# Kernel optimization log

Hardware: AMD Instinct MI355X
Metric: run time of the kernel (lower is better)

## Reference

```python
import jax, jax.numpy as jnp
import numpy as np
from jax import lax

N = 50000
E = 320000
IN_DIM = 128
OUT_DIM = 64
N_CHANNEL = 8
KERNEL = 3
N_REL = 500
BN_EPS = 1e-5


def setup_inputs() -> dict:
    key = jax.random.key(0)
    ks = jax.random.split(key, 10)
    inp = jax.random.normal(ks[0], (N, IN_DIM), dtype=jnp.float32)
    heads = jax.random.randint(ks[1], (E,), 0, N)
    rels = jax.random.randint(ks[2], (E,), 0, N_REL)
    tails = jax.random.randint(ks[3], (E,), 0, N)
    triple = jnp.stack([heads, rels, tails], axis=1).astype(jnp.int64)
    # parameters
    limit_W = float(np.sqrt(6.0 / (IN_DIM + OUT_DIM)))  # xavier_uniform
    W = jax.random.uniform(ks[4], (IN_DIM, OUT_DIM), minval=-limit_W, maxval=limit_W, dtype=jnp.float32)
    rel_embed = jax.random.normal(ks[5], (N_REL, OUT_DIM), dtype=jnp.float32)
    fan_in = 1 * KERNEL * KERNEL
    b = float(1.0 / np.sqrt(fan_in))
    conv_w = jax.random.uniform(ks[6], (N_CHANNEL, 1, KERNEL, KERNEL), minval=-b, maxval=b, dtype=jnp.float32)
    conv_b = jax.random.uniform(ks[7], (N_CHANNEL,), minval=-b, maxval=b, dtype=jnp.float32)
    fc_in = N_CHANNEL * (OUT_DIM - KERNEL + 1) * (3 - KERNEL + 1)
    bf = float(1.0 / np.sqrt(fc_in))
    fc_w = jax.random.uniform(ks[8], (1, fc_in), minval=-bf, maxval=bf, dtype=jnp.float32)
    bn1_gamma = jnp.ones((1,), jnp.float32)
    bn1_beta = jnp.zeros((1,), jnp.float32)
    bn2_gamma = jnp.ones((N_CHANNEL,), jnp.float32)
    bn2_beta = jnp.zeros((N_CHANNEL,), jnp.float32)
    return {"input": inp, "triple": triple, "W": W, "rel_embed": rel_embed,
            "conv_w": conv_w, "conv_b": conv_b, "fc_w": fc_w,
            "bn1_gamma": bn1_gamma, "bn1_beta": bn1_beta,
            "bn2_gamma": bn2_gamma, "bn2_beta": bn2_beta}


def _bn_eval(x, gamma, beta):
    # eval-mode BatchNorm with running_mean=0, running_var=1
    scale = gamma / jnp.sqrt(1.0 + BN_EPS)
    return x * scale.reshape(1, -1, 1, 1) + beta.reshape(1, -1, 1, 1)


def reference(input, triple, W, rel_embed, conv_w, conv_b, fc_w,
              bn1_gamma, bn1_beta, bn2_gamma, bn2_beta):
    n = input.shape[0]
    inp = input @ W                       # [N, out_dim]
    head = triple[:, 0]
    tail = triple[:, 2]
    h = inp[head]                         # [E, D]
    r = rel_embed[triple[:, 1]]           # [E, D]
    t = inp[tail]                         # [E, D]
    # energy function: [E,1,D,3] -> bn1 -> conv -> bn2 -> relu -> fc
    x = jnp.stack([h, r, t], axis=-1)[:, None, :, :]   # [E,1,D,3]
    x = _bn_eval(x, bn1_gamma, bn1_beta)
    y = lax.conv_general_dilated(x, conv_w, (1, 1), 'VALID',
                                 dimension_numbers=('NCHW', 'OIHW', 'NCHW'))
    y = y + conv_b.reshape(1, -1, 1, 1)                 # [E,C,D-2,1]
    y = jax.nn.relu(_bn_eval(y, bn2_gamma, bn2_beta))
    y = y.reshape(y.shape[0], -1)
    e = y @ fc_w[0]                                     # [E]
    e = jax.nn.leaky_relu(e, 0.01)
    # sparse softmax over rows (head) then sparse mm with input_
    m = jax.ops.segment_max(e, head, num_segments=n)
    ex = jnp.exp(e - m[head])
    denom = jax.ops.segment_sum(ex, head, num_segments=n)
    attn = ex / denom[head]
    agg = jax.ops.segment_sum(attn[:, None] * t, head, num_segments=n)
    return jax.nn.elu(agg + inp)
```

## Files before the change

kernel.cpp:

```cpp
#include <hip/hip_runtime.h>
#include <hip/hip_bf16.h>
#include <stdint.h>

#define IN_DIM   128
#define OUT_DIM  64
#define NCH      8
#define N_REL    500
#define BN_EPS   1e-5f
#define CAP      32


#define KEEP(x) asm volatile("" : "+v"(x))

__device__ __forceinline__ float dpp_shl1(float x) {
    return __int_as_float(__builtin_amdgcn_update_dpp(
        0, __float_as_int(x), 0x130, 0xf, 0xf, true));
}

__device__ __forceinline__ void fold_cw_thread(
    const float* __restrict__ conv_w, const float* __restrict__ conv_b,
    const float* __restrict__ bn1g, const float* __restrict__ bn1b,
    const float* __restrict__ bn2g, const float* __restrict__ bn2b,
    float* __restrict__ cw, int c)
{
    if (c >= NCH) return;
    float rs  = rsqrtf(1.f + BN_EPS);
    float s1  = bn1g[0] * rs;
    float be1 = bn1b[0];
    float s2  = bn2g[c] * rs;
    float k1  = s1 * s2;
    float wsum = 0.f;
    for (int d = 0; d < 3; ++d) {
        float a  = conv_w[c * 9 + d * 3 + 0];
        float b  = conv_w[c * 9 + d * 3 + 1];
        float cc = conv_w[c * 9 + d * 3 + 2];
        wsum += a + b + cc;
        cw[c * 3 + d]      = k1 * a;
        cw[24 + c * 3 + d] = k1 * b;
        cw[48 + c * 3 + d] = k1 * cc;
    }
    cw[72 + c] = (be1 * wsum + conv_b[c]) * s2 + bn2b[c];
}

__global__ __launch_bounds__(256) void k_build(
    const float* __restrict__ X, const float* __restrict__ W,
    const int* __restrict__ triple,
    const float* __restrict__ conv_w, const float* __restrict__ conv_b,
    const float* __restrict__ bn1g, const float* __restrict__ bn1b,
    const float* __restrict__ bn2g, const float* __restrict__ bn2b,
    float* __restrict__ inp, int* __restrict__ cnt, int2* __restrict__ rt32,
    float* __restrict__ cw, int E, int N, int ngemm)
{
    __shared__ float Wl[IN_DIM * OUT_DIM];
    __shared__ float Xl[32 * IN_DIM];

    if ((int)blockIdx.x < ngemm) {
        const int rows0 = blockIdx.x * 32;
        const float4* W4 = (const float4*)W;
        for (int i = threadIdx.x; i < IN_DIM * OUT_DIM / 4; i += 256)
            ((float4*)Wl)[i] = W4[i];
        for (int i = threadIdx.x; i < 32 * IN_DIM / 4; i += 256) {
            int r = i >> 5, k4 = i & 31;
            int rr = rows0 + r;
            float4 v = make_float4(0.f, 0.f, 0.f, 0.f);
            if (rr < N) v = ((const float4*)X)[(unsigned)rr * (IN_DIM / 4) + k4];
            ((float4*)Xl)[i] = v;
        }
        __syncthreads();

        const int w = threadIdx.x >> 6;
        const int c = threadIdx.x & 63;
        float acc[8];
        #pragma unroll
        for (int r = 0; r < 8; ++r) acc[r] = 0.f;

        for (int k4 = 0; k4 < IN_DIM / 4; ++k4) {
            int k = k4 * 4;
            float w0 = Wl[(k + 0) * OUT_DIM + c];
            float w1 = Wl[(k + 1) * OUT_DIM + c];
            float w2 = Wl[(k + 2) * OUT_DIM + c];
            float w3 = Wl[(k + 3) * OUT_DIM + c];
            #pragma unroll
            for (int r = 0; r < 8; ++r) {
                const float4 x = *(const float4*)&Xl[(w * 8 + r) * IN_DIM + k];
                acc[r] = fmaf(x.w, w3, fmaf(x.z, w2, fmaf(x.y, w1, fmaf(x.x, w0, acc[r]))));
            }
        }
        #pragma unroll
        for (int r = 0; r < 8; ++r) {
            int rr = rows0 + w * 8 + r;
            if (rr < N) inp[(unsigned)rr * OUT_DIM + c] = acc[r];
        }
    } else {
        const int bb   = blockIdx.x - ngemm;
        const int gtid = bb * 256 + threadIdx.x;
        if (bb == 0 && threadIdx.x < NCH)
            fold_cw_thread(conv_w, conv_b, bn1g, bn1b, bn2g, bn2b, cw, threadIdx.x);
        if (gtid < E) {
            int j = gtid;
            int h = triple[3 * j], r = triple[3 * j + 1], t = triple[3 * j + 2];
            h = min(max(h, 0), N - 1);
            r = min(max(r, 0), N_REL - 1);
            t = min(max(t, 0), N - 1);
            int pos = atomicAdd(&cnt[h], 1);
            if (pos < CAP) rt32[(unsigned)h * CAP + pos] = make_int2(r, t);
        }
    }
}

__device__ __forceinline__ float dpp_wave_sum(float x) {
    x += __int_as_float(__builtin_amdgcn_update_dpp(0, __float_as_int(x), 0x111, 0xf, 0xf, true));
    x += __int_as_float(__builtin_amdgcn_update_dpp(0, __float_as_int(x), 0x112, 0xf, 0xf, true));
    x += __int_as_float(__builtin_amdgcn_update_dpp(0, __float_as_int(x), 0x114, 0xf, 0xf, true));
    x += __int_as_float(__builtin_amdgcn_update_dpp(0, __float_as_int(x), 0x118, 0xf, 0xf, true));
    x += __int_as_float(__builtin_amdgcn_update_dpp(0, __float_as_int(x), 0x142, 0xf, 0xf, true));
    x += __int_as_float(__builtin_amdgcn_update_dpp(0, __float_as_int(x), 0x143, 0xf, 0xf, true));
    return __int_as_float(__builtin_amdgcn_readlane(__float_as_int(x), 63));
}

__global__ __launch_bounds__(256) void k_fused_all(
    const float* __restrict__ inp, const float* __restrict__ rel_embed,
    const float* __restrict__ cw, const float* __restrict__ fc_w,
    const int* __restrict__ cnt, const int2* __restrict__ rt32,
    float* __restrict__ out, int N)
{
    const int lane   = threadIdx.x & 63;
    const int wave   = (blockIdx.x * (blockDim.x >> 6)) + (threadIdx.x >> 6);
    const int nwaves = gridDim.x * (blockDim.x >> 6);

    float fcl[NCH];
    #pragma unroll
    for (int c = 0; c < NCH; ++c) {
        fcl[c] = (lane < 62) ? fc_w[c * 62 + lane] : 0.f;
        KEEP(fcl[c]);
    }

    for (int h = wave; h < N; h += nwaves) {
        const int deg = min(cnt[h], CAP);

        float h0 = inp[(unsigned)h * OUT_DIM + lane];
        float h1 = dpp_shl1(h0);
        float h2 = dpp_shl1(h1);
        float Ht[NCH];
        #pragma unroll
        for (int c = 0; c < NCH; ++c) {
            float v = cw[72 + c];
            v = fmaf(cw[c * 3 + 0], h0, v);
            v = fmaf(cw[c * 3 + 1], h1, v);
            v = fmaf(cw[c * 3 + 2], h2, v);
            Ht[c] = v;
            KEEP(Ht[c]);
        }

        float m_run = -INFINITY, l_run = 0.f, agg = 0.f;
        int2 rtv = make_int2(0, 0);
        if (lane < deg) rtv = rt32[(unsigned)h * CAP + lane];

        if (deg > 0) {
            int rk = __builtin_amdgcn_readlane(rtv.x, 0);
            int tk = __builtin_amdgcn_readlane(rtv.y, 0);
            float rr = rel_embed[(unsigned)rk * OUT_DIM + lane];
            float tt = inp      [(unsigned)tk * OUT_DIM + lane];

            for (int k = 0; k < deg; ++k) {
                int rk1 = __builtin_amdgcn_readlane(rtv.x, k + 1);
                int tk1 = __builtin_amdgcn_readlane(rtv.y, k + 1);
                float rrN = rel_embed[(unsigned)rk1 * OUT_DIM + lane];
                float ttN = inp      [(unsigned)tk1 * OUT_DIM + lane];

                float r1 = dpp_shl1(rr), r2 = dpp_shl1(r1);
                float t1 = dpp_shl1(tt), t2 = dpp_shl1(t1);

                float acc = 0.f;
                #pragma unroll
                for (int c = 0; c < NCH; ++c) {
                    float y = Ht[c];
                    y = fmaf(cw[24 + c * 3 + 0], rr, y);
                    y = fmaf(cw[24 + c * 3 + 1], r1, y);
                    y = fmaf(cw[24 + c * 3 + 2], r2, y);
                    y = fmaf(cw[48 + c * 3 + 0], tt, y);
                    y = fmaf(cw[48 + c * 3 + 1], t1, y);
                    y = fmaf(cw[48 + c * 3 + 2], t2, y);
                    acc = fmaf(fmaxf(y, 0.f), fcl[c], acc);
                }
                float s  = dpp_wave_sum(acc);
                float ev = fmaxf(s, 0.01f * s);

                float mn = fmaxf(m_run, ev);
                float sc = __expf(m_run - mn);
                float wk = __expf(ev - mn);
                agg   = fmaf(agg, sc, wk * tt);
                l_run = fmaf(l_run, sc, wk);
                m_run = mn;

                rr = rrN; tt = ttN;
            }
        }
        float aggn = (l_run > 0.f) ? agg / l_run : 0.f;
        float x = aggn + h0;
        float y = x > 0.f ? x : (__expf(x) - 1.f);
        out[(unsigned)h * OUT_DIM + lane] = y;
    }
}

extern "C" void kernel_launch(void* const* d_in, const int* in_sizes, int n_in,
                              void* d_out, int out_size, void* d_ws, size_t ws_size,
                              hipStream_t stream)
{
    const float* input     = (const float*)d_in[0];
    const int*   triple    = (const int*)d_in[1];
    const float* W         = (const float*)d_in[2];
    const float* rel_embed = (const float*)d_in[3];
    const float* conv_w    = (const float*)d_in[4];
    const float* conv_b    = (const float*)d_in[5];
    const float* fc_w      = (const float*)d_in[6];
    const float* bn1g      = (const float*)d_in[7];
    const float* bn1b      = (const float*)d_in[8];
    const float* bn2g      = (const float*)d_in[9];
    const float* bn2b      = (const float*)d_in[10];
    float*       out       = (float*)d_out;

    const int N = in_sizes[0] / IN_DIM;
    const int E = in_sizes[1] / 3;

    auto align = [](size_t x) { return (x + 255) & ~(size_t)255; };
    char* base = (char*)d_ws;
    size_t o = 0;
    float* inp  = (float*)(base + o); o = align(o + (size_t)N * OUT_DIM * 4);
    int2*  rt32 = (int2*)(base + o);  o = align(o + (size_t)N * CAP * 8);
    float* cw   = (float*)(base + o); o = align(o + 80 * 4);
    int*   cnt  = (int*)(base + o);   o = align(o + (size_t)N * 4);

    hipMemsetAsync(cnt, 0, (size_t)N * 4, stream);

    const int ngemm   = (N + 31) / 32;
    const int nbucket = (E + 255) / 256;
    k_build<<<ngemm + nbucket, 256, 0, stream>>>(
        input, W, triple, conv_w, conv_b, bn1g, bn1b, bn2g, bn2b,
        inp, cnt, rt32, cw, E, N, ngemm);

    const int nblk = (N + 3) / 4;
    k_fused_all<<<nblk, 256, 0, stream>>>(inp, rel_embed, cw, fc_w,
                                          cnt, rt32, out, N);
}
```

Before: 197.2 us.

## Precompute per-relation conv contributions table and double-buffer edge loads

Adds extra blocks to the build kernel that precompute, for each of the 500 relations, the 8-channel conv response of the relation embedding, so the edge loop no longer does 24 FMAs and 2 DPP shifts per edge for the relation column. The fused kernel instead reads two float4 values per lane from this 1 MB table. Conv weights are hoisted into scalar registers once per wave, and the edge loop is reworked into a two-slot software pipeline with two accumulators. Each edge now reads 8x more relation data, though the table is small enough to likely stay in cache, and register pressure rises.

```diff
diff --git a/kernel.cpp b/kernel.cpp
--- a/kernel.cpp
+++ b/kernel.cpp
@@ -15,6 +15,10 @@
 __device__ __forceinline__ float dpp_shl1(float x) {
     return __int_as_float(__builtin_amdgcn_update_dpp(
         0, __float_as_int(x), 0x130, 0xf, 0xf, true));
+}
+
+__device__ __forceinline__ float sget(float x) {
+    return __int_as_float(__builtin_amdgcn_readfirstlane(__float_as_int(x)));
 }
 
 __device__ __forceinline__ void fold_cw_thread(
@@ -44,12 +48,13 @@
 
 __global__ __launch_bounds__(256) void k_build(
     const float* __restrict__ X, const float* __restrict__ W,
-    const int* __restrict__ triple,
+    const int* __restrict__ triple, const float* __restrict__ rel_embed,
     const float* __restrict__ conv_w, const float* __restrict__ conv_b,
     const float* __restrict__ bn1g, const float* __restrict__ bn1b,
     const float* __restrict__ bn2g, const float* __restrict__ bn2b,
     float* __restrict__ inp, int* __restrict__ cnt, int2* __restrict__ rt32,
-    float* __restrict__ cw, int E, int N, int ngemm)
+    float* __restrict__ cw, float* __restrict__ Rt,
+    int E, int N, int ngemm, int nbucket)
 {
     __shared__ float Wl[IN_DIM * OUT_DIM];
     __shared__ float Xl[32 * IN_DIM];
@@ -91,7 +96,7 @@
             int rr = rows0 + w * 8 + r;
             if (rr < N) inp[(unsigned)rr * OUT_DIM + c] = acc[r];
         }
-    } else {
+    } else if ((int)blockIdx.x < ngemm + nbucket) {
         const int bb   = blockIdx.x - ngemm;
         const int gtid = bb * 256 + threadIdx.x;
         if (bb == 0 && threadIdx.x < NCH)
@@ -105,6 +110,28 @@
             int pos = atomicAdd(&cnt[h], 1);
             if (pos < CAP) rt32[(unsigned)h * CAP + pos] = make_int2(r, t);
         }
+    } else {
+        const int rb  = blockIdx.x - ngemm - nbucket;
+        const int ln  = threadIdx.x & 63;
+        const int rel = rb * 4 + (threadIdx.x >> 6);
+        if (rel < N_REL) {
+            float rr = rel_embed[(unsigned)rel * OUT_DIM + ln];
+            float r1 = dpp_shl1(rr), r2 = dpp_shl1(r1);
+            float rs = rsqrtf(1.f + BN_EPS);
+            float s1 = bn1g[0] * rs;
+            float q[NCH];
+            #pragma unroll
+            for (int c = 0; c < NCH; ++c) {
+                float k1 = s1 * (bn2g[c] * rs);
+                float b0 = k1 * conv_w[c * 9 + 1];
+                float b1 = k1 * conv_w[c * 9 + 4];
+                float b2 = k1 * conv_w[c * 9 + 7];
+                q[c] = fmaf(b0, rr, fmaf(b1, r1, b2 * r2));
+            }
+            float4* dst = (float4*)&Rt[(unsigned)rel * (OUT_DIM * NCH) + ln * NCH];
+            dst[0] = make_float4(q[0], q[1], q[2], q[3]);
+            dst[1] = make_float4(q[4], q[5], q[6], q[7]);
+        }
     }
 }
 
@@ -119,7 +146,7 @@
 }
 
 __global__ __launch_bounds__(256) void k_fused_all(
-    const float* __restrict__ inp, const float* __restrict__ rel_embed,
+    const float* __restrict__ inp, const float* __restrict__ Rt,
     const float* __restrict__ cw, const float* __restrict__ fc_w,
     const int* __restrict__ cnt, const int2* __restrict__ rt32,
     float* __restrict__ out, int N)
@@ -127,6 +154,18 @@
     const int lane   = threadIdx.x & 63;
     const int wave   = (blockIdx.x * (blockDim.x >> 6)) + (threadIdx.x >> 6);
     const int nwaves = gridDim.x * (blockDim.x >> 6);
+
+    float cA0[NCH], cA1[NCH], cA2[NCH], cC0[NCH], cC1[NCH], cC2[NCH], k0c[NCH];
+    #pragma unroll
+    for (int c = 0; c < NCH; ++c) {
+        cA0[c] = sget(cw[c * 3 + 0]);
+        cA1[c] = sget(cw[c * 3 + 1]);
+        cA2[c] = sget(cw[c * 3 + 2]);
+        cC0[c] = sget(cw[48 + c * 3 + 0]);
+        cC1[c] = sget(cw[48 + c * 3 + 1]);
+        cC2[c] = sget(cw[48 + c * 3 + 2]);
+        k0c[c] = sget(cw[72 + c]);
+    }
 
     float fcl[NCH];
     #pragma unroll
@@ -144,10 +183,10 @@
         float Ht[NCH];
         #pragma unroll
         for (int c = 0; c < NCH; ++c) {
-            float v = cw[72 + c];
-            v = fmaf(cw[c * 3 + 0], h0, v);
-            v = fmaf(cw[c * 3 + 1], h1, v);
-            v = fmaf(cw[c * 3 + 2], h2, v);
+            float v = k0c[c];
+            v = fmaf(cA0[c], h0, v);
+            v = fmaf(cA1[c], h1, v);
+            v = fmaf(cA2[c], h2, v);
             Ht[c] = v;
             KEEP(Ht[c]);
         }
@@ -157,44 +196,54 @@
         if (lane < deg) rtv = rt32[(unsigned)h * CAP + lane];
 
         if (deg > 0) {
-            int rk = __builtin_amdgcn_readlane(rtv.x, 0);
-            int tk = __builtin_amdgcn_readlane(rtv.y, 0);
-            float rr = rel_embed[(unsigned)rk * OUT_DIM + lane];
-            float tt = inp      [(unsigned)tk * OUT_DIM + lane];
-
-            for (int k = 0; k < deg; ++k) {
-                int rk1 = __builtin_amdgcn_readlane(rtv.x, k + 1);
-                int tk1 = __builtin_amdgcn_readlane(rtv.y, k + 1);
-                float rrN = rel_embed[(unsigned)rk1 * OUT_DIM + lane];
-                float ttN = inp      [(unsigned)tk1 * OUT_DIM + lane];
-
-                float r1 = dpp_shl1(rr), r2 = dpp_shl1(r1);
-                float t1 = dpp_shl1(tt), t2 = dpp_shl1(t1);
-
-                float acc = 0.f;
-                #pragma unroll
-                for (int c = 0; c < NCH; ++c) {
-                    float y = Ht[c];
-                    y = fmaf(cw[24 + c * 3 + 0], rr, y);
-                    y = fmaf(cw[24 + c * 3 + 1], r1, y);
-                    y = fmaf(cw[24 + c * 3 + 2], r2, y);
-                    y = fmaf(cw[48 + c * 3 + 0], tt, y);
-                    y = fmaf(cw[48 + c * 3 + 1], t1, y);
-                    y = fmaf(cw[48 + c * 3 + 2], t2, y);
-                    acc = fmaf(fmaxf(y, 0.f), fcl[c], acc);
-                }
-                float s  = dpp_wave_sum(acc);
-                float ev = fmaxf(s, 0.01f * s);
-
-                float mn = fmaxf(m_run, ev);
-                float sc = __expf(m_run - mn);
-                float wk = __expf(ev - mn);
-                agg   = fmaf(agg, sc, wk * tt);
-                l_run = fmaf(l_run, sc, wk);
-                m_run = mn;
-
-                rr = rrN; tt = ttN;
+#define LOADE(KK, Q0, Q1, TT)                                                   \
+            {   int rkL = __builtin_amdgcn_readlane(rtv.x, (KK));               \
+                int tkL = __builtin_amdgcn_readlane(rtv.y, (KK));               \
+                const float4* qp = (const float4*)&Rt[(unsigned)rkL * (OUT_DIM * NCH) \
+                                                      + (unsigned)(lane * NCH)]; \
+                Q0 = qp[0]; Q1 = qp[1];                                         \
+                TT = inp[(unsigned)tkL * OUT_DIM + lane]; }
+
+#define CH1(c, QC, AX)                                                          \
+                { float y = Ht[c] + (QC);                                       \
+                  y = fmaf(cC0[c], ttv, y);                                     \
+                  y = fmaf(cC1[c], t1v, y);                                     \
+                  y = fmaf(cC2[c], t2v, y);                                     \
+                  AX = fmaf(fmaxf(y, 0.f), fcl[c], AX); }
+
+#define EDGEC(Q0, Q1, TT)                                                       \
+            {   const float ttv = (TT);                                         \
+                float t1v = dpp_shl1(ttv), t2v = dpp_shl1(t1v);                 \
+                float a0 = 0.f, a1 = 0.f;                                       \
+                CH1(0, (Q0).x, a0) CH1(1, (Q0).y, a1)                           \
+                CH1(2, (Q0).z, a0) CH1(3, (Q0).w, a1)                           \
+                CH1(4, (Q1).x, a0) CH1(5, (Q1).y, a1)                           \
+                CH1(6, (Q1).z, a0) CH1(7, (Q1).w, a1)                           \
+                float s  = dpp_wave_sum(a0 + a1);                               \
+                float ev = fmaxf(s, 0.01f * s);                                 \
+                float mn = fmaxf(m_run, ev);                                    \
+                float sc = __expf(m_run - mn);                                  \
+                float wk = __expf(ev - mn);                                     \
+                agg   = fmaf(agg, sc, wk * ttv);                                \
+                l_run = fmaf(l_run, sc, wk);                                    \
+                m_run = mn; }
+
+            float4 qa0, qa1, qb0, qb1;
+            float  tta, ttb;
+            LOADE(0, qa0, qa1, tta)
+            LOADE(1, qb0, qb1, ttb)
+            int k = 0;
+            while (true) {
+                EDGEC(qa0, qa1, tta)
+                if (++k >= deg) break;
+                LOADE(k + 1, qa0, qa1, tta)
+                EDGEC(qb0, qb1, ttb)
+                if (++k >= deg) break;
+                LOADE(k + 1, qb0, qb1, ttb)
             }
+#undef EDGEC
+#undef CH1
+#undef LOADE
         }
         float aggn = (l_run > 0.f) ? agg / l_run : 0.f;
         float x = aggn + h0;
@@ -230,16 +279,18 @@
     int2*  rt32 = (int2*)(base + o);  o = align(o + (size_t)N * CAP * 8);
     float* cw   = (float*)(base + o); o = align(o + 80 * 4);
     int*   cnt  = (int*)(base + o);   o = align(o + (size_t)N * 4);
+    float* Rt   = (float*)(base + o); o = align(o + (size_t)N_REL * OUT_DIM * NCH * 4);
 
     hipMemsetAsync(cnt, 0, (size_t)N * 4, stream);
 
     const int ngemm   = (N + 31) / 32;
     const int nbucket = (E + 255) / 256;
-    k_build<<<ngemm + nbucket, 256, 0, stream>>>(
-        input, W, triple, conv_w, conv_b, bn1g, bn1b, bn2g, bn2b,
-        inp, cnt, rt32, cw, E, N, ngemm);
+    const int ntab    = (N_REL + 3) / 4;
+    k_build<<<ngemm + nbucket + ntab, 256, 0, stream>>>(
+        input, W, triple, rel_embed, conv_w, conv_b, bn1g, bn1b, bn2g, bn2b,
+        inp, cnt, rt32, cw, Rt, E, N, ngemm, nbucket);
 
     const int nblk = (N + 3) / 4;
-    k_fused_all<<<nblk, 256, 0, stream>>>(inp, rel_embed, cw, fc_w,
+    k_fused_all<<<nblk, 256, 0, stream>>>(inp, Rt, cw, fc_w,
                                           cnt, rt32, out, N);
 }
```

After: 185.6 us. 5.9% less time.
